# Kernel tuning notes

Measured on AMD Instinct MI355X. Metric: run time of the kernel, lower is better.

The kernel has to match this reference:

```python
import jax, jax.numpy as jnp
import numpy as np

B, T, D, H, K, V, W = 2, 2048, 768, 12, 64, 64, 1024
EPS = 1e-6


def setup_inputs() -> dict:
    key = jax.random.key(0)
    ks = jax.random.split(key, 10)
    std = 0.02
    return {
        "x": jax.random.normal(ks[0], (B, T, D), jnp.float32),
        "gdn_state": jax.random.normal(ks[1], (B, H, K, V), jnp.float32),
        "Wq": jax.random.normal(ks[2], (D, H * K), jnp.float32) * std,
        "Wk": jax.random.normal(ks[3], (D, H * K), jnp.float32) * std,
        "Wv": jax.random.normal(ks[4], (D, H * K), jnp.float32) * std,
        "Wo": jax.random.normal(ks[5], (H * K, D), jnp.float32) * std,
        "Wgq": jax.random.normal(ks[6], (D, H * K), jnp.float32) * std,
        "Wro": jax.random.normal(ks[7], (H * V, D), jnp.float32) * std,
        "Wg": jax.random.normal(ks[8], (D, H), jnp.float32) * std,
        "bg": jnp.full((H,), 1.0, jnp.float32),  # swa_gate_init
        "norm_w": jnp.ones((D,), jnp.float32),
    }


def reference(x, gdn_state, Wq, Wk, Wv, Wo, Wgq, Wro, Wg, bg, norm_w):
    # RMSNorm
    xn = x * jax.lax.rsqrt(jnp.mean(x * x, axis=-1, keepdims=True) + EPS) * norm_w

    def proj(w):  # (B,T,D)@(D,HK) -> (B,H,T,K)
        return (xn @ w).reshape(B, T, H, K).transpose(0, 2, 1, 3)

    q, k, v = proj(Wq), proj(Wk), proj(Wv)
    scale = K ** -0.5

    scores = jnp.einsum("bhqk,bhsk->bhqs", q, k) * scale  # (B,H,T,T)
    i = jnp.arange(T)[:, None]
    j = jnp.arange(T)[None, :]
    allowed = (j <= i) & (j >= i - W)  # causal sliding window
    scores = jnp.where(allowed, scores, -jnp.inf)
    attn = jax.nn.softmax(scores, axis=-1)

    local = jnp.einsum("bhqs,bhsk->bhqk", attn, v)
    local = local.transpose(0, 2, 1, 3).reshape(B, T, H * K) @ Wo  # (B,T,D)

    # GDN state retrieval
    qg = jax.nn.relu((xn @ Wgq).reshape(B, T, H, K).transpose(0, 2, 1, 3))  # (B,H,T,K)
    retrieved = jnp.einsum("bhkv,bhtk->bhtv", gdn_state, qg)  # (B,H,T,V)
    retrieval = retrieved.transpose(0, 2, 1, 3).reshape(B, T, H * V) @ Wro  # (B,T,D)
    gate = jax.nn.sigmoid(xn @ Wg + bg)  # (B,T,H)
    retrieval = jnp.mean(gate, axis=-1, keepdims=True) * retrieval

    return x + local + retrieval
```

## Files before the change

kernel.cpp:

```cpp
#include <hip/hip_runtime.h>
#include <math.h>
#include <stdint.h>

typedef float f32x4 __attribute__((ext_vector_type(4)));
typedef __bf16 bf16x8 __attribute__((ext_vector_type(8)));
typedef __bf16 bf16x4 __attribute__((ext_vector_type(4)));

constexpr int Bc = 2, Tc = 2048, Dc = 768, Hc = 12, Wc = 1024;
#define CEXP 0.18033688011112042f

__device__ __forceinline__ f32x4 mfma_bf16(bf16x8 a, bf16x8 b, f32x4 c) {
    return __builtin_amdgcn_mfma_f32_16x16x32_bf16(a, b, c, 0, 0, 0);
}
__device__ __forceinline__ void gload16(const void* g, void* l) {
    __builtin_amdgcn_global_load_lds(
        (const __attribute__((address_space(1))) uint32_t*)g,
        (__attribute__((address_space(3))) uint32_t*)l, 16, 0, 0);
}
__device__ __forceinline__ uint32_t pack2(float a, float b) {
    union { __bf16 h[2]; uint32_t u; } x;
    x.h[0] = (__bf16)a; x.h[1] = (__bf16)b; return x.u;
}

__global__ __launch_bounds__(256) void k_prep_w(
    const float* __restrict__ Wq, const float* __restrict__ Wk,
    const float* __restrict__ Wv, const float* __restrict__ Wgq,
    const float* __restrict__ Wo, const float* __restrict__ Wro,
    __bf16* __restrict__ wTproj, __bf16* __restrict__ wTout)
{
    __shared__ __bf16 ldsT[64][66];
    const int wsel = blockIdx.y;
    const float* srcs[6] = {Wq, Wk, Wv, Wgq, Wo, Wro};
    const float* src = srcs[wsel];
    __bf16* dst; int dstride, koff;
    if (wsel < 4) { dst = wTproj + (size_t)wsel * Dc * Dc; dstride = Dc;  koff = 0; }
    else if (wsel == 4) { dst = wTout; dstride = 1536; koff = 0; }
    else { dst = wTout; dstride = 1536; koff = 768; }
    const float scale = (wsel == 0) ? CEXP : 1.0f;

    int tile = blockIdx.x;
    int tk = tile % 12, tn = tile / 12;
    int k0 = tk * 64, n0 = tn * 64;
    int i = threadIdx.x, rsub = i >> 4, c4 = i & 15;
#pragma unroll
    for (int rep = 0; rep < 4; ++rep) {
        int row = rep * 16 + rsub;
        float4 v = *(const float4*)(src + (size_t)(k0 + row) * Dc + n0 + c4 * 4);
        ldsT[c4 * 4 + 0][row] = (__bf16)(v.x * scale);
        ldsT[c4 * 4 + 1][row] = (__bf16)(v.y * scale);
        ldsT[c4 * 4 + 2][row] = (__bf16)(v.z * scale);
        ldsT[c4 * 4 + 3][row] = (__bf16)(v.w * scale);
    }
    __syncthreads();
#pragma unroll
    for (int rep = 0; rep < 4; ++rep) {
        int n = rep * 16 + rsub;
        bf16x4 o = *(const bf16x4*)&ldsT[n][c4 * 4];
        *(bf16x4*)(dst + (size_t)(n0 + n) * dstride + koff + k0 + c4 * 4) = o;
    }
}

__global__ __launch_bounds__(256) void k_prep_state(
    const float* __restrict__ st, __bf16* __restrict__ stT)
{
    int idx = blockIdx.x * 256 + threadIdx.x;
    int bh = idx >> 12, kk = (idx >> 6) & 63, vv = idx & 63;
    stT[(size_t)bh * 4096 + vv * 64 + kk] = (__bf16)st[idx];
}

__global__ __launch_bounds__(256) void k_rmsnorm(
    const float* __restrict__ x, const float* __restrict__ norm_w,
    __bf16* __restrict__ xnb)
{
    int row = blockIdx.x, tid = threadIdx.x;
    const float* xr = x + (size_t)row * Dc;
    float4 v = make_float4(0.f, 0.f, 0.f, 0.f);
    float ss = 0.f;
    if (tid < 192) {
        v = ((const float4*)xr)[tid];
        ss = v.x * v.x + v.y * v.y + v.z * v.z + v.w * v.w;
    }
#pragma unroll
    for (int m = 32; m; m >>= 1) ss += __shfl_xor(ss, m, 64);
    __shared__ float red[4];
    if ((tid & 63) == 0) red[tid >> 6] = ss;
    __syncthreads();
    float tot = red[0] + red[1] + red[2] + red[3];
    float rms = rsqrtf(tot * (1.f / 768.f) + 1e-6f);
    if (tid < 192) {
        float4 nw = ((const float4*)norm_w)[tid];
        bf16x4 o;
        o[0] = (__bf16)(v.x * rms * nw.x);
        o[1] = (__bf16)(v.y * rms * nw.y);
        o[2] = (__bf16)(v.z * rms * nw.z);
        o[3] = (__bf16)(v.w * rms * nw.w);
        *(bf16x4*)(xnb + (size_t)row * Dc + tid * 4) = o;
    }
}

__global__ __launch_bounds__(256) void k_gate(
    const __bf16* __restrict__ xnb, const float* __restrict__ Wg,
    const float* __restrict__ bg, float* __restrict__ gmean)
{
    int row = blockIdx.x * 4 + (threadIdx.x >> 6);
    int lane = threadIdx.x & 63;
    const __bf16* xr = xnb + (size_t)row * Dc;
    float p[12];
#pragma unroll
    for (int h = 0; h < 12; ++h) p[h] = 0.f;
    for (int d = lane; d < Dc; d += 64) {
        float xv = (float)xr[d];
        const float* wr = Wg + d * 12;
#pragma unroll
        for (int h = 0; h < 12; ++h) p[h] += xv * wr[h];
    }
#pragma unroll
    for (int h = 0; h < 12; ++h) {
#pragma unroll
        for (int m = 32; m; m >>= 1) p[h] += __shfl_xor(p[h], m, 64);
    }
    if (lane == 0) {
        float s = 0.f;
#pragma unroll
        for (int h = 0; h < 12; ++h) s += 1.f / (1.f + expf(-(p[h] + bg[h])));
        gmean[row] = s * (1.f / 12.f);
    }
}

template <int MODE>
__global__ __launch_bounds__(256) void k_gemm(
    const __bf16* __restrict__ A, const __bf16* __restrict__ BT,
    const float* __restrict__ xres, float* __restrict__ outf,
    __bf16* __restrict__ qb, __bf16* __restrict__ kbf,
    __bf16* __restrict__ vtb, __bf16* __restrict__ qgb)
{
    constexpr int BM = (MODE == 0) ? 128 : 64;
    constexpr int BN = (MODE == 0) ? 128 : 64;
    constexpr int KD = (MODE == 0) ? 768 : 1536;
    constexpr int WM = BM / 2, WN = BN / 2;
    constexpr int MI = WM / 16, NI = WN / 16;
    constexpr int MT = 4096 / BM;
    __shared__ __bf16 As[BM * 64];
    __shared__ __bf16 Bs[BN * 64];
    const int tid = threadIdx.x, w = tid >> 6, lane = tid & 63;
    const int g = lane >> 4, t = lane & 15;
    int id = blockIdx.x, xcd = id & 7, l = id >> 3;
    int nid = xcd * 96 + l;
    int m0 = (nid % MT) * BM, n0 = (nid / MT) * BN;
    const __bf16* Abase = A + (size_t)m0 * KD;
    const __bf16* Bbase = BT + (size_t)n0 * KD;
    const int wrow = (w >> 1) * WM, wcol = (w & 1) * WN;
    const int xr = t & 7;

    f32x4 acc[MI][NI] = {};
    for (int k0 = 0; k0 < KD; k0 += 64) {
#pragma unroll
        for (int c = 0; c < BM / 32; ++c) {
            int chunk = c * 256 + tid, row = chunk >> 3, cix = chunk & 7;
            gload16(Abase + (size_t)row * KD + k0 + ((cix ^ (row & 7)) << 3),
                    As + chunk * 8);
        }
#pragma unroll
        for (int c = 0; c < BN / 32; ++c) {
            int chunk = c * 256 + tid, row = chunk >> 3, cix = chunk & 7;
            gload16(Bbase + (size_t)row * KD + k0 + ((cix ^ (row & 7)) << 3),
                    Bs + chunk * 8);
        }
        __syncthreads();
#pragma unroll
        for (int kk = 0; kk < 2; ++kk) {
            bf16x8 af[MI], bfr[NI];
#pragma unroll
            for (int mi = 0; mi < MI; ++mi)
                af[mi] = *(const bf16x8*)(As + (wrow + mi * 16 + t) * 64 +
                                          (((g + kk * 4) ^ xr) << 3));
#pragma unroll
            for (int ni = 0; ni < NI; ++ni)
                bfr[ni] = *(const bf16x8*)(Bs + (wcol + ni * 16 + t) * 64 +
                                           (((g + kk * 4) ^ xr) << 3));
#pragma unroll
            for (int mi = 0; mi < MI; ++mi)
#pragma unroll
                for (int ni = 0; ni < NI; ++ni)
                    acc[mi][ni] = mfma_bf16(af[mi], bfr[ni], acc[mi][ni]);
        }
        __syncthreads();
    }
    const int region = (MODE == 0) ? (n0 / 768) : 0;
#pragma unroll
    for (int mi = 0; mi < MI; ++mi)
#pragma unroll
        for (int ni = 0; ni < NI; ++ni)
#pragma unroll
            for (int r = 0; r < 4; ++r) {
                int grow = m0 + wrow + mi * 16 + g * 4 + r;
                int gcol = n0 + wcol + ni * 16 + t;
                float v = acc[mi][ni][r];
                if (MODE == 1) {
                    size_t idx = (size_t)grow * Dc + gcol;
                    outf[idx] = xres[idx] + v;
                } else {
                    int c = gcol - region * 768;
                    int h = c >> 6, kd = c & 63;
                    int b = grow >> 11, ti = grow & (Tc - 1);
                    if (region == 0)
                        qb[((size_t)(b * Hc + h) * Tc + ti) * 64 + kd] = (__bf16)v;
                    else if (region == 1) {
                        int kds = kd ^ ((ti & 7) << 3);
                        kbf[((size_t)(b * Hc + h) * Tc + ti) * 64 + kds] = (__bf16)v;
                    } else if (region == 2) {
                        int kap = ti & 63;
                        int rho = (kap & 32) | (((kap >> 2) & 3) << 3) |
                                  (((kap >> 4) & 1) << 2) | (kap & 3);
                        int ts = (ti & ~63) | (rho ^ ((kd & 7) << 3));
                        vtb[((size_t)(b * Hc + h) * 64 + kd) * Tc + ts] = (__bf16)v;
                    } else
                        qgb[((size_t)(b * Hc + h) * Tc + ti) * 64 + kd] = (__bf16)fmaxf(v, 0.f);
                }
            }
}

__global__ __launch_bounds__(256) void k_attn(
    const __bf16* __restrict__ q, const __bf16* __restrict__ k,
    const __bf16* __restrict__ vt, __bf16* __restrict__ ac)
{
    __shared__ __bf16 Ks[2][64 * 64];
    __shared__ __bf16 Vs[2][64 * 64];
    int id = blockIdx.x, xcd = id & 7, l = id >> 3;
    int nid = xcd * 96 + l;
    int sblk = nid & 31, h = (nid >> 5) % Hc, b = nid / (32 * Hc);
    int tid = threadIdx.x;
    int w = tid >> 6, lane = tid & 63;
    int g = lane >> 4, t = lane & 15;
    int q0 = sblk * 64, qw = q0 + w * 16;
    const __bf16* qb = q + (size_t)(b * Hc + h) * Tc * 64;
    const __bf16* kb = k + (size_t)(b * Hc + h) * Tc * 64;
    const __bf16* vb = vt + (size_t)(b * Hc + h) * 64 * Tc;

    bf16x8 qf0 = *(const bf16x8*)(qb + (size_t)(qw + t) * 64 + g * 8);
    bf16x8 qf1 = *(const bf16x8*)(qb + (size_t)(qw + t) * 64 + 32 + g * 8);

    const int qi = qw + t;
    const int lowB = qi - Wc;
    const int xr = t & 7;

    f32x4 oacc[4] = {};
    float lsum = 0.f;

    const int s_begin = (q0 >= Wc) ? q0 - Wc : 0;
    const int s_endq = q0 + 64;

    auto STAGE = [&](int buf, int s0) {
#pragma unroll
        for (int j = 0; j < 2; ++j) {
            int ch = j * 256 + tid;
            gload16(kb + (size_t)(s0 + (ch >> 3)) * 64 + (ch & 7) * 8,
                    &Ks[buf][ch * 8]);
            gload16(vb + (size_t)(ch >> 3) * Tc + s0 + (ch & 7) * 8,
                    &Vs[buf][ch * 8]);
        }
    };

    STAGE(0, s_begin);
    __syncthreads();
    int cur = 0;
    for (int s0 = s_begin; s0 < s_endq; s0 += 64) {
        if (s0 + 64 < s_endq) STAGE(cur ^ 1, s0 + 64);
        const __bf16* Kt = Ks[cur];
        const __bf16* Vt = Vs[cur];
        f32x4 sc[4];
#pragma unroll
        for (int sub = 0; sub < 4; ++sub) {
            const __bf16* kr = Kt + (sub * 16 + t) * 64;
            bf16x8 kA = *(const bf16x8*)(kr + ((g ^ xr) << 3));
            bf16x8 kB = *(const bf16x8*)(kr + (((g + 4) ^ xr) << 3));
            f32x4 s = {};
            s = mfma_bf16(kA, qf0, s);
            s = mfma_bf16(kB, qf1, s);
            sc[sub] = s;
        }
        float pv[4][4];
#pragma unroll
        for (int sub = 0; sub < 4; ++sub)
#pragma unroll
            for (int r = 0; r < 4; ++r) {
                int kk = s0 + sub * 16 + g * 4 + r;
                float e = exp2f(sc[sub][r]);
                float val = (kk <= qi && kk >= lowB) ? e : 0.f;
                pv[sub][r] = val;
                lsum += val;
            }
#pragma unroll
        for (int ks = 0; ks < 2; ++ks) {
            union { uint32_t u[4]; bf16x8 v; } pf;
            pf.u[0] = pack2(pv[ks * 2][0], pv[ks * 2][1]);
            pf.u[1] = pack2(pv[ks * 2][2], pv[ks * 2][3]);
            pf.u[2] = pack2(pv[ks * 2 + 1][0], pv[ks * 2 + 1][1]);
            pf.u[3] = pack2(pv[ks * 2 + 1][2], pv[ks * 2 + 1][3]);
#pragma unroll
            for (int n = 0; n < 4; ++n) {
                const __bf16* vrow = Vt + (n * 16 + t) * 64;
                bf16x8 vf = *(const bf16x8*)(vrow + ((((ks * 4) + g) ^ xr) << 3));
                oacc[n] = mfma_bf16(pf.v, vf, oacc[n]);
            }
        }
        __syncthreads();
        cur ^= 1;
    }
    lsum += __shfl_xor(lsum, 16, 64);
    lsum += __shfl_xor(lsum, 32, 64);
    float linv = 1.f / lsum;
    float lq[4];
#pragma unroll
    for (int r = 0; r < 4; ++r) lq[r] = __shfl(linv, g * 4 + r, 64);
#pragma unroll
    for (int n = 0; n < 4; ++n)
#pragma unroll
        for (int r = 0; r < 4; ++r) {
            int qrow = qw + g * 4 + r;
            ac[(size_t)(b * Tc + qrow) * 1536 + h * 64 + n * 16 + t] =
                (__bf16)(oacc[n][r] * lq[r]);
        }
}

__global__ __launch_bounds__(256) void k_retr(
    const __bf16* __restrict__ qg, const __bf16* __restrict__ stateT,
    const float* __restrict__ gmean, __bf16* __restrict__ ac)
{
    int b = blockIdx.z, h = blockIdx.y;
    int w = threadIdx.x >> 6, lane = threadIdx.x & 63;
    int g = lane >> 4, t = lane & 15;
    int t0 = blockIdx.x * 64 + w * 16;
    const __bf16* qbp = qg + (size_t)(b * Hc + h) * Tc * 64;
    const __bf16* sb = stateT + (size_t)(b * Hc + h) * 64 * 64;
    bf16x8 a0 = *(const bf16x8*)(qbp + (size_t)(t0 + t) * 64 + g * 8);
    bf16x8 a1 = *(const bf16x8*)(qbp + (size_t)(t0 + t) * 64 + 32 + g * 8);
#pragma unroll
    for (int n = 0; n < 4; ++n) {
        bf16x8 b0 = *(const bf16x8*)(sb + (n * 16 + t) * 64 + g * 8);
        bf16x8 b1 = *(const bf16x8*)(sb + (n * 16 + t) * 64 + 32 + g * 8);
        f32x4 acc = {};
        acc = mfma_bf16(a0, b0, acc);
        acc = mfma_bf16(a1, b1, acc);
#pragma unroll
        for (int r = 0; r < 4; ++r) {
            int ti = t0 + g * 4 + r;
            float gm = gmean[b * Tc + ti];
            ac[(size_t)(b * Tc + ti) * 1536 + 768 + h * 64 + n * 16 + t] =
                (__bf16)(acc[r] * gm);
        }
    }
}

extern "C" void kernel_launch(void* const* d_in, const int* in_sizes, int n_in,
                              void* d_out, int out_size, void* d_ws, size_t ws_size,
                              hipStream_t stream) {
    (void)in_sizes; (void)n_in; (void)out_size; (void)ws_size;
    const float* x     = (const float*)d_in[0];
    const float* gdn   = (const float*)d_in[1];
    const float* Wq    = (const float*)d_in[2];
    const float* Wk    = (const float*)d_in[3];
    const float* Wv    = (const float*)d_in[4];
    const float* Wo    = (const float*)d_in[5];
    const float* Wgq   = (const float*)d_in[6];
    const float* Wro   = (const float*)d_in[7];
    const float* Wg    = (const float*)d_in[8];
    const float* bg    = (const float*)d_in[9];
    const float* normw = (const float*)d_in[10];
    float* out = (float*)d_out;

    char* p = (char*)d_ws;
    auto alloc = [&](size_t bytes) -> char* {
        char* r = p; p += (bytes + 255) & ~(size_t)255; return r;
    };
    constexpr size_t NROW = (size_t)Bc * Tc;
    __bf16* xnb    = (__bf16*)alloc(NROW * Dc * 2);
    __bf16* wTproj = (__bf16*)alloc((size_t)4 * Dc * Dc * 2);
    __bf16* wTout  = (__bf16*)alloc((size_t)Dc * 1536 * 2);
    __bf16* stT    = (__bf16*)alloc((size_t)Bc * Hc * 64 * 64 * 2);
    __bf16* qbuf   = (__bf16*)alloc(NROW * Dc * 2);
    __bf16* kbuf   = (__bf16*)alloc(NROW * Dc * 2);
    __bf16* qgbuf  = (__bf16*)alloc(NROW * Dc * 2);
    __bf16* vtbuf  = (__bf16*)alloc(NROW * Dc * 2);
    __bf16* ac     = (__bf16*)alloc(NROW * 1536 * 2);
    float*  gmean  = (float*)alloc(NROW * 4);

    k_prep_w<<<dim3(144, 6), 256, 0, stream>>>(Wq, Wk, Wv, Wgq, Wo, Wro, wTproj, wTout);
    k_prep_state<<<(Bc * Hc * 64 * 64) / 256, 256, 0, stream>>>(gdn, stT);
    k_rmsnorm<<<NROW, 256, 0, stream>>>(x, normw, xnb);
    k_gate<<<NROW / 4, 256, 0, stream>>>(xnb, Wg, bg, gmean);

    k_gemm<0><<<768, 256, 0, stream>>>(xnb, wTproj, nullptr, nullptr,
                                       qbuf, kbuf, vtbuf, qgbuf);
    k_attn<<<768, 256, 0, stream>>>(qbuf, kbuf, vtbuf, ac);
    k_retr<<<dim3(Tc / 64, Hc, Bc), 256, 0, stream>>>(qgbuf, stT, gmean, ac);
    k_gemm<1><<<768, 256, 0, stream>>>(ac, wTout, x, out,
                                       nullptr, nullptr, nullptr, nullptr);
}
```

Before: 137.7 us.

## Double-buffer GEMM shared-memory tiles and prefetch next K slice during MFMA

The projection/output GEMM kernel now keeps two LDS buffers for the A and B tiles. It issues the global-to-LDS loads for the next K slice before computing on the current one, so load latency can overlap the MFMA work. The K tile shrinks to 32 for the large-tile mode to keep LDS usage in check. The XOR swizzle on LDS rows is dropped in favour of a plain row-major layout, which risks LDS bank conflicts on the fragment reads.

```diff
diff --git a/kernel.cpp b/kernel.cpp
--- a/kernel.cpp
+++ b/kernel.cpp
@@ -137,11 +137,16 @@
     constexpr int BM = (MODE == 0) ? 128 : 64;
     constexpr int BN = (MODE == 0) ? 128 : 64;
     constexpr int KD = (MODE == 0) ? 768 : 1536;
+    constexpr int BK = (MODE == 0) ? 32 : 64;
     constexpr int WM = BM / 2, WN = BN / 2;
     constexpr int MI = WM / 16, NI = WN / 16;
     constexpr int MT = 4096 / BM;
-    __shared__ __bf16 As[BM * 64];
-    __shared__ __bf16 Bs[BN * 64];
+    constexpr int NK = KD / BK;
+    constexpr int GR = BK / 8;
+    constexpr int ACH = BM * BK / 2048;
+    constexpr int BCH = BN * BK / 2048;
+    __shared__ __bf16 As[2][BM * BK];
+    __shared__ __bf16 Bs[2][BN * BK];
     const int tid = threadIdx.x, w = tid >> 6, lane = tid & 63;
     const int g = lane >> 4, t = lane & 15;
     int id = blockIdx.x, xcd = id & 7, l = id >> 3;
@@ -150,34 +155,36 @@
     const __bf16* Abase = A + (size_t)m0 * KD;
     const __bf16* Bbase = BT + (size_t)n0 * KD;
     const int wrow = (w >> 1) * WM, wcol = (w & 1) * WN;
-    const int xr = t & 7;
+
+    auto STAGE = [&](int buf, int k0) {
+#pragma unroll
+        for (int c = 0; c < ACH; ++c) {
+            int chunk = c * 256 + tid, row = chunk / GR, cix = chunk % GR;
+            gload16(Abase + (size_t)row * KD + k0 + cix * 8, &As[buf][chunk * 8]);
+        }
+#pragma unroll
+        for (int c = 0; c < BCH; ++c) {
+            int chunk = c * 256 + tid, row = chunk / GR, cix = chunk % GR;
+            gload16(Bbase + (size_t)row * KD + k0 + cix * 8, &Bs[buf][chunk * 8]);
+        }
+    };
 
     f32x4 acc[MI][NI] = {};
-    for (int k0 = 0; k0 < KD; k0 += 64) {
-#pragma unroll
-        for (int c = 0; c < BM / 32; ++c) {
-            int chunk = c * 256 + tid, row = chunk >> 3, cix = chunk & 7;
-            gload16(Abase + (size_t)row * KD + k0 + ((cix ^ (row & 7)) << 3),
-                    As + chunk * 8);
-        }
-#pragma unroll
-        for (int c = 0; c < BN / 32; ++c) {
-            int chunk = c * 256 + tid, row = chunk >> 3, cix = chunk & 7;
-            gload16(Bbase + (size_t)row * KD + k0 + ((cix ^ (row & 7)) << 3),
-                    Bs + chunk * 8);
-        }
-        __syncthreads();
-#pragma unroll
-        for (int kk = 0; kk < 2; ++kk) {
+    STAGE(0, 0);
+    __syncthreads();
+    for (int ks = 0; ks < NK; ++ks) {
+        if (ks + 1 < NK) STAGE((ks + 1) & 1, (ks + 1) * BK);
+        const __bf16* Ab = As[ks & 1];
+        const __bf16* Bb = Bs[ks & 1];
+#pragma unroll
+        for (int kk = 0; kk < BK / 32; ++kk) {
             bf16x8 af[MI], bfr[NI];
 #pragma unroll
             for (int mi = 0; mi < MI; ++mi)
-                af[mi] = *(const bf16x8*)(As + (wrow + mi * 16 + t) * 64 +
-                                          (((g + kk * 4) ^ xr) << 3));
+                af[mi] = *(const bf16x8*)(Ab + (wrow + mi * 16 + t) * BK + kk * 32 + g * 8);
 #pragma unroll
             for (int ni = 0; ni < NI; ++ni)
-                bfr[ni] = *(const bf16x8*)(Bs + (wcol + ni * 16 + t) * 64 +
-                                           (((g + kk * 4) ^ xr) << 3));
+                bfr[ni] = *(const bf16x8*)(Bb + (wcol + ni * 16 + t) * BK + kk * 32 + g * 8);
 #pragma unroll
             for (int mi = 0; mi < MI; ++mi)
 #pragma unroll
```

After: 141.7 us. 2.9% more time.
